# Performance work log

Measured on AMD Instinct MI355X. Metric: run time of the kernel, lower is better.

The kernel has to match this reference:

```python
import jax, jax.numpy as jnp
import numpy as np

N = 1_000_000
C = 32
GRID_SIZE = (16, 16, 16, 16, 16)

# Only 4 corners are combined in the original module: dims 0 and 1 vary
# between floor/ceil, dims 2-4 always use floor.
CORNER_OFFSETS = np.array([
    [0, 0, 0, 0, 0],
    [1, 0, 0, 0, 0],
    [0, 1, 0, 0, 0],
    [1, 1, 0, 0, 0],
], dtype=np.int32)  # (4, 5)


def setup_inputs() -> dict:
    key = jax.random.key(0)
    k1, k2 = jax.random.split(key)
    ray = jax.random.uniform(k1, (N, 5), dtype=jnp.float32)
    grid = jax.random.normal(k2, (1, C) + GRID_SIZE, dtype=jnp.float32)
    ray_min = jnp.zeros((5,), dtype=jnp.float32)
    ray_max = jnp.ones((5,), dtype=jnp.float32)
    return {"ray": ray, "grid": grid, "ray_min": ray_min, "ray_max": ray_max}


def reference(ray, grid, ray_min, ray_max):
    dims = np.array(grid.shape[2:], dtype=np.int64)       # (D0..D4)
    C_ = grid.shape[1]
    P = int(np.prod(dims))
    strides = np.array([np.prod(dims[i + 1:]) for i in range(5)], dtype=np.int32)  # (5,)

    # Normalize ray -> fractional grid coordinates, shape (N, 5)
    ind = (ray - ray_min) / (ray_max - ray_min) * (dims.astype(np.float32) - 1.0)
    bottom = jnp.floor(ind).astype(jnp.int32)              # (N, 5)
    w = ind - bottom.astype(ind.dtype)                     # (N, 5) interp weights

    offs = jnp.asarray(CORNER_OFFSETS)                     # (4, 5)
    corner = bottom[None, :, :] + offs[:, None, :]         # (4, N, 5)

    dims_j = jnp.asarray(dims.astype(np.int32))
    valid = jnp.all((corner >= 0) & (corner < dims_j), axis=-1)          # (4, N)
    lin = jnp.sum(corner * jnp.asarray(strides), axis=-1)                # (4, N)
    lin = jnp.clip(lin, 0, P - 1)

    # Per-corner multilinear weights: pick w where offset==1 else (1-w), product over 5 dims
    wsel = jnp.where(offs[:, None, :] == 1, w[None, :, :], 1.0 - w[None, :, :])  # (4, N, 5)
    comb_w = jnp.prod(wsel, axis=-1) * valid.astype(ind.dtype)                   # (4, N)

    grid_flat = grid.reshape(C_, P)                        # (C, P)
    vals = grid_flat[:, lin]                               # (C, 4, N) gather
    out = jnp.einsum('cfn,fn->nc', vals, comb_w)           # (N, C)
    return out
```

## Files before the change

kernel.cpp:

```cpp
#include <hip/hip_runtime.h>
#include <hip/hip_fp16.h>

#define PCELLS (16*16*16*16*16)
#define CCH 32

struct Corner { int4 lin; float4 w; };

__device__ __forceinline__ void ray_corners(const float* __restrict__ ray,
                                            const float* __restrict__ mn,
                                            const float* __restrict__ mx,
                                            int n, int* lin, float* wt) {
    float w[5]; int b[5];
#pragma unroll
    for (int d = 0; d < 5; ++d) {
        float r   = ray[(size_t)n * 5 + d];
        float t   = (r - mn[d]) / (mx[d] - mn[d]);
        float ind = t * 15.0f;
        float fb  = floorf(ind);
        b[d] = (int)fb;
        w[d] = ind - fb;
    }
    bool vrest = (b[2] >= 0) & (b[2] < 16) & (b[3] >= 0) & (b[3] < 16) &
                 (b[4] >= 0) & (b[4] < 16);
    float tau = (1.f - w[2]) * (1.f - w[3]) * (1.f - w[4]);
    if (!vrest) tau = 0.f;
    int rest = b[2] * 256 + b[3] * 16 + b[4];

    bool v0l = (b[0] >= 0) & (b[0] < 16);
    bool v0h = (b[0] + 1 >= 0) & (b[0] + 1 < 16);
    bool v1l = (b[1] >= 0) & (b[1] < 16);
    bool v1h = (b[1] + 1 >= 0) & (b[1] + 1 < 16);
    float w0 = w[0], w1 = w[1];

    wt[0] = (1.f - w0) * (1.f - w1) * tau * ((v0l & v1l) ? 1.f : 0.f);
    wt[1] = w0 * (1.f - w1) * tau * ((v0h & v1l) ? 1.f : 0.f);
    wt[2] = (1.f - w0) * w1 * tau * ((v0l & v1h) ? 1.f : 0.f);
    wt[3] = w0 * w1 * tau * ((v0h & v1h) ? 1.f : 0.f);

    int l00 = b[0] * 65536 + b[1] * 4096 + rest;
    int lv[4] = { l00, l00 + 65536, l00 + 4096, l00 + 65536 + 4096 };
#pragma unroll
    for (int f = 0; f < 4; ++f)
        lin[f] = min(max(lv[f], 0), PCELLS - 1);
}

__global__ __launch_bounds__(256) void transpose_kernel(
        const float* __restrict__ g, __half* __restrict__ gt) {
    __shared__ float tile[CCH][64 + 1];
    const int p0 = blockIdx.x * 64;
    const int t  = threadIdx.x;

#pragma unroll
    for (int i = 0; i < 8; ++i) {
        int f = t + i * 256;
        int c = f >> 6;
        int p = f & 63;
        tile[c][p] = g[(size_t)c * PCELLS + p0 + p];
    }
    __syncthreads();
#pragma unroll
    for (int i = 0; i < 4; ++i) {
        int f  = t + i * 256;
        int p  = f >> 4;
        int c2 = f & 15;
        __half2 h;
        h.x = __float2half(tile[2 * c2][p]);
        h.y = __float2half(tile[2 * c2 + 1][p]);
        ((__half2*)gt)[(size_t)(p0 + p) * 16 + c2];
        ((__half2*)gt)[(size_t)(p0 + p) * 16 + c2] = h;
    }
}

__global__ __launch_bounds__(256) void prep_kernel(
        const float* __restrict__ ray, const float* __restrict__ mn,
        const float* __restrict__ mx, Corner* __restrict__ corners, int N) {
    int n = blockIdx.x * blockDim.x + threadIdx.x;
    if (n >= N) return;
    int lin[4]; float wt[4];
    ray_corners(ray, mn, mx, n, lin, wt);
    Corner cn;
    cn.lin = make_int4(lin[0], lin[1], lin[2], lin[3]);
    cn.w   = make_float4(wt[0], wt[1], wt[2], wt[3]);
    corners[n] = cn;
}

__global__ __launch_bounds__(256) void gather_kernel(
        const __half* __restrict__ gt, const Corner* __restrict__ corners,
        float* __restrict__ out, int N) {
    int tid = blockIdx.x * blockDim.x + threadIdx.x;
    int n = tid >> 5;
    int c = tid & 31;
    if (n >= N) return;
    Corner cn = corners[n];
    float acc = cn.w.x * __half2float(gt[(size_t)cn.lin.x * CCH + c])
              + cn.w.y * __half2float(gt[(size_t)cn.lin.y * CCH + c])
              + cn.w.z * __half2float(gt[(size_t)cn.lin.z * CCH + c])
              + cn.w.w * __half2float(gt[(size_t)cn.lin.w * CCH + c]);
    out[(size_t)n * CCH + c] = acc;
}

__global__ __launch_bounds__(256) void direct_kernel(
        const float* __restrict__ ray, const float* __restrict__ g,
        const float* __restrict__ mn, const float* __restrict__ mx,
        float* __restrict__ out, int N) {
    int tid = blockIdx.x * blockDim.x + threadIdx.x;
    int n = tid >> 5;
    int c = tid & 31;
    if (n >= N) return;
    int lin[4]; float wt[4];
    ray_corners(ray, mn, mx, n, lin, wt);
    const float* gc = g + (size_t)c * PCELLS;
    float acc = wt[0] * gc[lin[0]] + wt[1] * gc[lin[1]] +
                wt[2] * gc[lin[2]] + wt[3] * gc[lin[3]];
    out[(size_t)n * CCH + c] = acc;
}

extern "C" void kernel_launch(void* const* d_in, const int* in_sizes, int n_in,
                              void* d_out, int out_size, void* d_ws, size_t ws_size,
                              hipStream_t stream) {
    const float* ray  = (const float*)d_in[0];
    const float* grid = (const float*)d_in[1];
    const float* mn   = (const float*)d_in[2];
    const float* mx   = (const float*)d_in[3];
    float* out = (float*)d_out;
    const int N = in_sizes[0] / 5;

    const size_t gt_bytes = (size_t)PCELLS * CCH * sizeof(__half);
    const size_t cn_bytes = (size_t)N * sizeof(Corner);

    if (ws_size >= gt_bytes + cn_bytes) {
        __half* gt      = (__half*)d_ws;
        Corner* corners = (Corner*)((char*)d_ws + gt_bytes);

        transpose_kernel<<<PCELLS / 64, 256, 0, stream>>>(grid, gt);
        prep_kernel<<<(N + 255) / 256, 256, 0, stream>>>(ray, mn, mx, corners, N);
        long long total = (long long)N * CCH;
        gather_kernel<<<(int)((total + 255) / 256), 256, 0, stream>>>(gt, corners, out, N);
    } else {
        long long total = (long long)N * CCH;
        direct_kernel<<<(int)((total + 255) / 256), 256, 0, stream>>>(ray, grid, mn, mx, out, N);
    }
}
```

Baseline: 346.4 us.

## Fuse corner prep into gather, vectorize transpose and half2 channel loads

Removes the separate prep kernel and its corner buffer, so each gather thread recomputes the ray corners and weights itself. Each thread now handles two rays and one half2 channel pair (16 threads per ray), using vector half2 loads and float2 stores. The transpose kernel switches to 128-cell tiles with float4 global loads and 16-byte stores of packed halves. The trade is redundant per-thread ray arithmetic and scattered ray reads in exchange for less intermediate memory traffic and one fewer launch.

Result: faster. 324.4 us (-6.3%).

```diff
diff --git a/kernel.cpp b/kernel.cpp
--- a/kernel.cpp
+++ b/kernel.cpp
@@ -3,8 +3,7 @@
 
 #define PCELLS (16*16*16*16*16)
 #define CCH 32
-
-struct Corner { int4 lin; float4 w; };
+#define TILE_P 128
 
 __device__ __forceinline__ void ray_corners(const float* __restrict__ ray,
                                             const float* __restrict__ mn,
@@ -46,57 +45,73 @@
 
 __global__ __launch_bounds__(256) void transpose_kernel(
         const float* __restrict__ g, __half* __restrict__ gt) {
-    __shared__ float tile[CCH][64 + 1];
-    const int p0 = blockIdx.x * 64;
+    __shared__ float tile[CCH][TILE_P + 4];
+    const int p0 = blockIdx.x * TILE_P;
     const int t  = threadIdx.x;
 
 #pragma unroll
-    for (int i = 0; i < 8; ++i) {
-        int f = t + i * 256;
-        int c = f >> 6;
-        int p = f & 63;
-        tile[c][p] = g[(size_t)c * PCELLS + p0 + p];
+    for (int i = 0; i < 4; ++i) {
+        int idx = t + i * 256;
+        int c   = idx >> 5;
+        int q   = idx & 31;
+        const float4 v = *(const float4*)(g + (size_t)c * PCELLS + p0 + 4 * q);
+        *(float4*)&tile[c][4 * q] = v;
     }
     __syncthreads();
+
 #pragma unroll
-    for (int i = 0; i < 4; ++i) {
-        int f  = t + i * 256;
-        int p  = f >> 4;
-        int c2 = f & 15;
-        __half2 h;
-        h.x = __float2half(tile[2 * c2][p]);
-        h.y = __float2half(tile[2 * c2 + 1][p]);
-        ((__half2*)gt)[(size_t)(p0 + p) * 16 + c2];
-        ((__half2*)gt)[(size_t)(p0 + p) * 16 + c2] = h;
+    for (int i = 0; i < 2; ++i) {
+        int idx = t + i * 256;
+        int p   = idx >> 2;
+        int k   = idx & 3;
+        __half2 h[4];
+#pragma unroll
+        for (int j = 0; j < 4; ++j) {
+            h[j] = __floats2half2_rn(tile[8 * k + 2 * j][p],
+                                     tile[8 * k + 2 * j + 1][p]);
+        }
+        *(float4*)(gt + (size_t)(p0 + p) * CCH + 8 * k) = *(float4*)h;
     }
 }
 
-__global__ __launch_bounds__(256) void prep_kernel(
-        const float* __restrict__ ray, const float* __restrict__ mn,
-        const float* __restrict__ mx, Corner* __restrict__ corners, int N) {
-    int n = blockIdx.x * blockDim.x + threadIdx.x;
-    if (n >= N) return;
-    int lin[4]; float wt[4];
-    ray_corners(ray, mn, mx, n, lin, wt);
-    Corner cn;
-    cn.lin = make_int4(lin[0], lin[1], lin[2], lin[3]);
-    cn.w   = make_float4(wt[0], wt[1], wt[2], wt[3]);
-    corners[n] = cn;
-}
-
-__global__ __launch_bounds__(256) void gather_kernel(
-        const __half* __restrict__ gt, const Corner* __restrict__ corners,
+__global__ __launch_bounds__(256) void fused_gather(
+        const float* __restrict__ ray, const __half2* __restrict__ gt2,
+        const float* __restrict__ mn, const float* __restrict__ mx,
         float* __restrict__ out, int N) {
     int tid = blockIdx.x * blockDim.x + threadIdx.x;
-    int n = tid >> 5;
-    int c = tid & 31;
-    if (n >= N) return;
-    Corner cn = corners[n];
-    float acc = cn.w.x * __half2float(gt[(size_t)cn.lin.x * CCH + c])
-              + cn.w.y * __half2float(gt[(size_t)cn.lin.y * CCH + c])
-              + cn.w.z * __half2float(gt[(size_t)cn.lin.z * CCH + c])
-              + cn.w.w * __half2float(gt[(size_t)cn.lin.w * CCH + c]);
-    out[(size_t)n * CCH + c] = acc;
+    int pr  = tid >> 4;
+    int c2  = tid & 15;
+    int n0  = 2 * pr;
+    if (n0 >= N) return;
+    bool has1 = (n0 + 1) < N;
+    int n1 = has1 ? (n0 + 1) : n0;
+
+    int   lin0[4], lin1[4];
+    float wt0[4],  wt1[4];
+    ray_corners(ray, mn, mx, n0, lin0, wt0);
+    ray_corners(ray, mn, mx, n1, lin1, wt1);
+
+    __half2 v0[4], v1[4];
+#pragma unroll
+    for (int f = 0; f < 4; ++f) v0[f] = gt2[(size_t)lin0[f] * 16 + c2];
+#pragma unroll
+    for (int f = 0; f < 4; ++f) v1[f] = gt2[(size_t)lin1[f] * 16 + c2];
+
+    float2 a0 = make_float2(0.f, 0.f), a1 = make_float2(0.f, 0.f);
+#pragma unroll
+    for (int f = 0; f < 4; ++f) {
+        float2 x = __half22float2(v0[f]);
+        a0.x += wt0[f] * x.x;  a0.y += wt0[f] * x.y;
+    }
+#pragma unroll
+    for (int f = 0; f < 4; ++f) {
+        float2 x = __half22float2(v1[f]);
+        a1.x += wt1[f] * x.x;  a1.y += wt1[f] * x.y;
+    }
+
+    *(float2*)(out + (size_t)n0 * CCH + 2 * c2) = a0;
+    if (has1)
+        *(float2*)(out + (size_t)n1 * CCH + 2 * c2) = a1;
 }
 
 __global__ __launch_bounds__(256) void direct_kernel(
@@ -126,18 +141,18 @@
     const int N = in_sizes[0] / 5;
 
     const size_t gt_bytes = (size_t)PCELLS * CCH * sizeof(__half);
-    const size_t cn_bytes = (size_t)N * sizeof(Corner);
 
-    if (ws_size >= gt_bytes + cn_bytes) {
-        __half* gt      = (__half*)d_ws;
-        Corner* corners = (Corner*)((char*)d_ws + gt_bytes);
+    if (ws_size >= gt_bytes) {
+        __half* gt = (__half*)d_ws;
+        transpose_kernel<<<PCELLS / TILE_P, 256, 0, stream>>>(grid, gt);
 
-        transpose_kernel<<<PCELLS / 64, 256, 0, stream>>>(grid, gt);
-        prep_kernel<<<(N + 255) / 256, 256, 0, stream>>>(ray, mn, mx, corners, N);
-        long long total = (long long)N * CCH;
-        gather_kernel<<<(int)((total + 255) / 256), 256, 0, stream>>>(gt, corners, out, N);
+        long long pairs   = (N + 1) / 2;
+        long long threads = pairs * 16;
+        fused_gather<<<(int)((threads + 255) / 256), 256, 0, stream>>>(
+            ray, (const __half2*)gt, mn, mx, out, N);
     } else {
         long long total = (long long)N * CCH;
-        direct_kernel<<<(int)((total + 255) / 256), 256, 0, stream>>>(ray, grid, mn, mx, out, N);
+        direct_kernel<<<(int)((total + 255) / 256), 256, 0, stream>>>(
+            ray, grid, mn, mx, out, N);
     }
 }
```
